# Optimization experiments

Hardware: AMD Instinct MI355X
Metric: run time of the kernel (lower is better)

## Reference

```python
import jax, jax.numpy as jnp
import numpy as np

F = 16      # frames
NV = 4096   # visual points per frame
NT = 512    # tactile points per frame
M = 4096    # model points
SCALE = 0.1


def setup_inputs() -> dict:
    key = jax.random.key(0)
    ks = jax.random.split(key, 6)
    return {
        "state": jax.random.normal(ks[0], (6,), dtype=jnp.float32) * 0.1,
        "model_points": jax.random.normal(ks[1], (M, 3), dtype=jnp.float32),
        "visual_points": jax.random.normal(ks[2], (F, NV, 3), dtype=jnp.float32),
        "tactile_points": jax.random.normal(ks[3], (F, NT, 3), dtype=jnp.float32),
        "physics_pred_states": jax.random.normal(ks[4], (F, 12), dtype=jnp.float32) * 0.1,
        "delta_time": jax.random.uniform(ks[5], (F,), dtype=jnp.float32, minval=0.01, maxval=0.05),
    }


def _skew(a):
    z = jnp.zeros((), a.dtype)
    return jnp.array([[z, -a[2], a[1]],
                      [a[2], z, -a[0]],
                      [-a[1], a[0], z]])


def _rot_from_omega(omega, dt):
    # Rodrigues: R = I + sin(theta*dt) S + (1 - cos(theta*dt)) S@S, S = skew(omega/|omega|)
    theta = jnp.linalg.norm(omega)
    ax = omega / jnp.clip(theta, 1e-8)
    S = _skew(ax)
    return jnp.eye(3, dtype=omega.dtype) + jnp.sin(theta * dt) * S + (1.0 - jnp.cos(theta * dt)) * (S @ S)


def _chamfer(pred, gt):
    # rows: pred [N,3], cols: gt [M,3]; row-min of squared distances, then mean
    d = (jnp.sum(pred * pred, axis=1)[:, None]
         + jnp.sum(gt * gt, axis=1)[None, :]
         - 2.0 * pred @ gt.T)
    return jnp.mean(jnp.min(d, axis=1))


def reference(state, model_points, visual_points, tactile_points, physics_pred_states, delta_time):
    t0 = state[:3]
    r0 = _rot_from_omega(state[3:], jnp.float32(1.0))  # Euler2Mat modeled as axis-angle

    def pose_step(carry, x):
        t, r = carry
        v, omega, dt = x
        t = t + v * dt
        r = _rot_from_omega(omega, dt) @ r
        return (t, r), (t, r)

    _, (ts, rs) = jax.lax.scan(
        pose_step, (t0, r0),
        (physics_pred_states[1:, 6:9], physics_pred_states[1:, 9:12], delta_time[1:]))
    ts = jnp.concatenate([t0[None], ts], axis=0)  # [F,3]
    rs = jnp.concatenate([r0[None], rs], axis=0)  # [F,3,3]

    def frame_loss(acc, x):
        t, r, vp, tp = x
        vc = ((vp - t) @ r) / SCALE
        tc = ((tp - t) @ r) / SCALE
        acc = acc + _chamfer(vc, model_points) + 0.1 * _chamfer(tc, model_points)
        return acc, None

    E_cd, _ = jax.lax.scan(frame_loss, jnp.zeros((), jnp.float32),
                           (ts, rs, visual_points, tactile_points))
    return E_cd
```

## Files before the change

kernel.cpp:

```cpp
#include <hip/hip_runtime.h>
#include <math.h>

#define F_    16
#define NV_   4096
#define NT_   512
#define M_    4096
#define PPF_  (NV_ + NT_)
#define NPTS_ (F_ * PPF_)
#define SCALE_INV 10.0f

#define TPB    256
#define NPB    36
#define NCHUNK 32
#define CPM    128
#define PPT    8

#define PART_OFF (72 * 1024)

typedef float v2f __attribute__((ext_vector_type(2)));

__device__ inline void rot_from_omega(float ox, float oy, float oz, float dt,
                                      float* R) {
    float theta = sqrtf(ox * ox + oy * oy + oz * oz);
    float inv = 1.0f / fmaxf(theta, 1e-8f);
    float ax = ox * inv, ay = oy * inv, az = oz * inv;
    float s = sinf(theta * dt);
    float c = 1.0f - cosf(theta * dt);
    R[0] = 1.0f - c * (ay * ay + az * az);
    R[1] = -s * az + c * ax * ay;
    R[2] =  s * ay + c * ax * az;
    R[3] =  s * az + c * ax * ay;
    R[4] = 1.0f - c * (ax * ax + az * az);
    R[5] = -s * ax + c * ay * az;
    R[6] = -s * ay + c * ax * az;
    R[7] =  s * ax + c * ay * az;
    R[8] = 1.0f - c * (ax * ax + ay * ay);
}

__device__ __forceinline__ void pkdist2(v2f qa01, v2f qa23, v2f qb01, v2f qb23,
                                        const v2f* c0, const v2f* c1,
                                        const v2f* c2, float* dm) {
    v2f A0, A1, A2, A3, B0, B1, B2, B3;
    asm(
        "v_pk_fma_f32 %0, %9, %20, %9  op_sel:[0,0,1] op_sel_hi:[0,1,1]\n\t"
        "v_pk_fma_f32 %1, %9, %21, %9  op_sel:[0,0,1] op_sel_hi:[0,1,1]\n\t"
        "v_pk_fma_f32 %2, %9, %22, %9  op_sel:[0,0,1] op_sel_hi:[0,1,1]\n\t"
        "v_pk_fma_f32 %3, %9, %23, %9  op_sel:[0,0,1] op_sel_hi:[0,1,1]\n\t"
        "v_pk_fma_f32 %4, %11, %20, %11 op_sel:[0,0,1] op_sel_hi:[0,1,1]\n\t"
        "v_pk_fma_f32 %5, %11, %21, %11 op_sel:[0,0,1] op_sel_hi:[0,1,1]\n\t"
        "v_pk_fma_f32 %6, %11, %22, %11 op_sel:[0,0,1] op_sel_hi:[0,1,1]\n\t"
        "v_pk_fma_f32 %7, %11, %23, %11 op_sel:[0,0,1] op_sel_hi:[0,1,1]\n\t"
        "v_pk_fma_f32 %0, %8, %16, %0  op_sel:[1,0,0] op_sel_hi:[1,1,1]\n\t"
        "v_pk_fma_f32 %1, %8, %17, %1  op_sel:[1,0,0] op_sel_hi:[1,1,1]\n\t"
        "v_pk_fma_f32 %2, %8, %18, %2  op_sel:[1,0,0] op_sel_hi:[1,1,1]\n\t"
        "v_pk_fma_f32 %3, %8, %19, %3  op_sel:[1,0,0] op_sel_hi:[1,1,1]\n\t"
        "v_pk_fma_f32 %4, %10, %16, %4 op_sel:[1,0,0] op_sel_hi:[1,1,1]\n\t"
        "v_pk_fma_f32 %5, %10, %17, %5 op_sel:[1,0,0] op_sel_hi:[1,1,1]\n\t"
        "v_pk_fma_f32 %6, %10, %18, %6 op_sel:[1,0,0] op_sel_hi:[1,1,1]\n\t"
        "v_pk_fma_f32 %7, %10, %19, %7 op_sel:[1,0,0] op_sel_hi:[1,1,1]\n\t"
        "v_pk_fma_f32 %0, %8, %12, %0  op_sel:[0,0,0] op_sel_hi:[0,1,1]\n\t"
        "v_pk_fma_f32 %1, %8, %13, %1  op_sel:[0,0,0] op_sel_hi:[0,1,1]\n\t"
        "v_pk_fma_f32 %2, %8, %14, %2  op_sel:[0,0,0] op_sel_hi:[0,1,1]\n\t"
        "v_pk_fma_f32 %3, %8, %15, %3  op_sel:[0,0,0] op_sel_hi:[0,1,1]\n\t"
        "v_pk_fma_f32 %4, %10, %12, %4 op_sel:[0,0,0] op_sel_hi:[0,1,1]\n\t"
        "v_pk_fma_f32 %5, %10, %13, %5 op_sel:[0,0,0] op_sel_hi:[0,1,1]\n\t"
        "v_pk_fma_f32 %6, %10, %14, %6 op_sel:[0,0,0] op_sel_hi:[0,1,1]\n\t"
        "v_pk_fma_f32 %7, %10, %15, %7 op_sel:[0,0,0] op_sel_hi:[0,1,1]"
        : "=&v"(A0), "=&v"(A1), "=&v"(A2), "=&v"(A3),
          "=&v"(B0), "=&v"(B1), "=&v"(B2), "=&v"(B3)
        : "s"(qa01), "s"(qa23), "s"(qb01), "s"(qb23),
          "v"(c0[0]), "v"(c0[1]), "v"(c0[2]), "v"(c0[3]),
          "v"(c1[0]), "v"(c1[1]), "v"(c1[2]), "v"(c1[3]),
          "v"(c2[0]), "v"(c2[1]), "v"(c2[2]), "v"(c2[3]));
    dm[0] = fminf(fminf(A0.x, B0.x), dm[0]);
    dm[1] = fminf(fminf(A0.y, B0.y), dm[1]);
    dm[2] = fminf(fminf(A1.x, B1.x), dm[2]);
    dm[3] = fminf(fminf(A1.y, B1.y), dm[3]);
    dm[4] = fminf(fminf(A2.x, B2.x), dm[4]);
    dm[5] = fminf(fminf(A2.y, B2.y), dm[5]);
    dm[6] = fminf(fminf(A3.x, B3.x), dm[6]);
    dm[7] = fminf(fminf(A3.y, B3.y), dm[7]);
}

__global__ void prep_kernel(const float* __restrict__ state,
                            const float* __restrict__ phys,
                            const float* __restrict__ dts,
                            const float* __restrict__ model,
                            float* __restrict__ ws_pose,
                            float4* __restrict__ ws_feat) {
    const int b = blockIdx.x, t = threadIdx.x;
    if (b == 0) {
        __shared__ float sRs[F_ * 9];
        __shared__ float sdt[F_ * 3];
        if (t < F_) {
            float ox, oy, oz, dt;
            if (t == 0) { ox = state[3]; oy = state[4]; oz = state[5]; dt = 1.0f; }
            else        { ox = phys[t * 12 + 9]; oy = phys[t * 12 + 10];
                          oz = phys[t * 12 + 11]; dt = dts[t]; }
            float Rs[9];
            rot_from_omega(ox, oy, oz, dt, Rs);
            for (int j = 0; j < 9; ++j) sRs[t * 9 + j] = Rs[j];
            if (t > 0) {
                sdt[t * 3 + 0] = phys[t * 12 + 6] * dt;
                sdt[t * 3 + 1] = phys[t * 12 + 7] * dt;
                sdt[t * 3 + 2] = phys[t * 12 + 8] * dt;
            }
        }
        if (t == 0) {
            float R[9];
            for (int j = 0; j < 9; ++j) R[j] = sRs[j];
            float tr[3] = {state[0], state[1], state[2]};
            for (int i = 0; i < F_; ++i) {
                if (i > 0) {
                    tr[0] += sdt[i * 3 + 0];
                    tr[1] += sdt[i * 3 + 1];
                    tr[2] += sdt[i * 3 + 2];
                    float Rn[9];
                    const float* Rsp = sRs + i * 9;
                    for (int r = 0; r < 3; ++r)
                        for (int c2 = 0; c2 < 3; ++c2)
                            Rn[r * 3 + c2] = Rsp[r * 3 + 0] * R[0 + c2] +
                                             Rsp[r * 3 + 1] * R[3 + c2] +
                                             Rsp[r * 3 + 2] * R[6 + c2];
                    for (int j = 0; j < 9; ++j) R[j] = Rn[j];
                }
                float* o = ws_pose + i * 12;
                o[0] = tr[0]; o[1] = tr[1]; o[2] = tr[2];
                for (int j = 0; j < 9; ++j) o[3 + j] = R[j] * SCALE_INV;
            }
        }
    } else {
        const int id = (b - 1) * 256 + t;
        float gx = model[id * 3 + 0], gy = model[id * 3 + 1], gz = model[id * 3 + 2];
        ws_feat[id] = make_float4(-2.0f * gx, -2.0f * gy, -2.0f * gz,
                                  gx * gx + gy * gy + gz * gz);
    }
}

__global__ __launch_bounds__(TPB, 4) void chamfer_main(
    const float* __restrict__ vis, const float* __restrict__ tac,
    const float* __restrict__ ws_pose, const float4* __restrict__ ws_feat,
    float* __restrict__ partials) {
    __shared__ float spose[F_ * 12];
    const int t  = threadIdx.x;
    const int pb = blockIdx.x;
    const int ch = blockIdx.y;

    if (t < F_ * 12) spose[t] = ws_pose[t];
    __syncthreads();

    v2f c0p[4], c1p[4], c2p[4];
    float cn[PPT], dm[PPT];
#pragma unroll
    for (int k = 0; k < PPT; ++k) {
        int pt  = pb * 2048 + k * 256 + t;
        int f   = pt / PPF_;
        int loc = pt - f * PPF_;
        const float* p = (loc < NV_) ? (vis + ((size_t)f * NV_ + loc) * 3)
                                     : (tac + ((size_t)f * NT_ + (loc - NV_)) * 3);
        const float* ps = spose + f * 12;
        float d0 = p[0] - ps[0], d1 = p[1] - ps[1], d2 = p[2] - ps[2];
        const float* R = ps + 3;
        float x = d0 * R[0] + d1 * R[3] + d2 * R[6];
        float y = d0 * R[1] + d1 * R[4] + d2 * R[7];
        float z = d0 * R[2] + d1 * R[5] + d2 * R[8];
        cn[k] = x * x + y * y + z * z;
        dm[k] = 3.4e38f;
        if (k & 1) { c0p[k >> 1].y = x; c1p[k >> 1].y = y; c2p[k >> 1].y = z; }
        else       { c0p[k >> 1].x = x; c1p[k >> 1].x = y; c2p[k >> 1].x = z; }
    }

    const v2f* fch = (const v2f*)(ws_feat + (size_t)ch * CPM);
#pragma unroll 4
    for (int m = 0; m < CPM; m += 2) {
        v2f qa01 = fch[2 * m + 0];
        v2f qa23 = fch[2 * m + 1];
        v2f qb01 = fch[2 * m + 2];
        v2f qb23 = fch[2 * m + 3];
        pkdist2(qa01, qa23, qb01, qb23, c0p, c1p, c2p, dm);
    }

#pragma unroll
    for (int k = 0; k < PPT; ++k)
        partials[(size_t)ch * NPTS_ + pb * 2048 + k * 256 + t] = dm[k] + cn[k];
}

__global__ __launch_bounds__(TPB) void chamfer_reduce(
    const float* __restrict__ partials, float* __restrict__ out) {
    __shared__ float sw[TPB / 64];
    const int pt = blockIdx.x * TPB + threadIdx.x;
    float m = partials[pt];
    for (int ch = 1; ch < NCHUNK; ++ch)
        m = fminf(m, partials[(size_t)ch * NPTS_ + pt]);
    const int loc = pt % PPF_;
    const float w = (loc < NV_) ? (1.0f / NV_) : (0.1f / NT_);
    float v = m * w;
#pragma unroll
    for (int off = 32; off > 0; off >>= 1) v += __shfl_down(v, off);
    if ((threadIdx.x & 63) == 0) sw[threadIdx.x >> 6] = v;
    __syncthreads();
    if (threadIdx.x == 0) {
        float s = 0.0f;
        for (int i = 0; i < TPB / 64; ++i) s += sw[i];
        atomicAdd(out, s);
    }
}

__global__ __launch_bounds__(TPB) void chamfer_fb(
    const float* __restrict__ state, const float* __restrict__ model,
    const float* __restrict__ vis, const float* __restrict__ tac,
    const float* __restrict__ phys, const float* __restrict__ dts,
    float* __restrict__ out) {
    __shared__ float sw[4];
    const int pt = blockIdx.x * TPB + threadIdx.x;
    const int f = pt / PPF_, loc = pt - f * PPF_;
    float R[9], tr[3] = {state[0], state[1], state[2]};
    rot_from_omega(state[3], state[4], state[5], 1.0f, R);
    for (int i = 1; i <= f; ++i) {
        float dt = dts[i];
        tr[0] += phys[i * 12 + 6] * dt;
        tr[1] += phys[i * 12 + 7] * dt;
        tr[2] += phys[i * 12 + 8] * dt;
        float Rs[9], Rn[9];
        rot_from_omega(phys[i * 12 + 9], phys[i * 12 + 10], phys[i * 12 + 11], dt, Rs);
        for (int r = 0; r < 3; ++r)
            for (int c2 = 0; c2 < 3; ++c2)
                Rn[r * 3 + c2] = Rs[r * 3 + 0] * R[0 + c2] +
                                 Rs[r * 3 + 1] * R[3 + c2] +
                                 Rs[r * 3 + 2] * R[6 + c2];
        for (int j = 0; j < 9; ++j) R[j] = Rn[j];
    }
    for (int j = 0; j < 9; ++j) R[j] *= SCALE_INV;
    const float* p = (loc < NV_) ? (vis + ((size_t)f * NV_ + loc) * 3)
                                 : (tac + ((size_t)f * NT_ + (loc - NV_)) * 3);
    float d0 = p[0] - tr[0], d1 = p[1] - tr[1], d2 = p[2] - tr[2];
    float x = d0 * R[0] + d1 * R[3] + d2 * R[6];
    float y = d0 * R[1] + d1 * R[4] + d2 * R[7];
    float z = d0 * R[2] + d1 * R[5] + d2 * R[8];
    float cn = x * x + y * y + z * z;
    float mn = 3.4e38f;
    for (int i = 0; i < M_; ++i) {
        float gx = model[i * 3], gy = model[i * 3 + 1], gz = model[i * 3 + 2];
        float gn = gx * gx + gy * gy + gz * gz;
        float dd = fmaf(-2.0f * gx, x, fmaf(-2.0f * gy, y, fmaf(-2.0f * gz, z, gn)));
        mn = fminf(mn, dd);
    }
    float w = (loc < NV_) ? (1.0f / NV_) : (0.1f / NT_);
    float v = (mn + cn) * w;
    for (int off = 32; off > 0; off >>= 1) v += __shfl_down(v, off);
    if ((threadIdx.x & 63) == 0) sw[threadIdx.x >> 6] = v;
    __syncthreads();
    if (threadIdx.x == 0) atomicAdd(out, sw[0] + sw[1] + sw[2] + sw[3]);
}

extern "C" void kernel_launch(void* const* d_in, const int* in_sizes, int n_in,
                              void* d_out, int out_size, void* d_ws, size_t ws_size,
                              hipStream_t stream) {
    const float* state = (const float*)d_in[0];
    const float* model = (const float*)d_in[1];
    const float* vis   = (const float*)d_in[2];
    const float* tac   = (const float*)d_in[3];
    const float* phys  = (const float*)d_in[4];
    const float* dts   = (const float*)d_in[5];
    float* out = (float*)d_out;

    const size_t NEED = PART_OFF + (size_t)NCHUNK * NPTS_ * sizeof(float);
    hipMemsetAsync(out, 0, sizeof(float), stream);
    if (ws_size >= NEED) {
        float*  ws_pose  = (float*)d_ws;
        float4* ws_feat  = (float4*)((char*)d_ws + 1024);
        float*  partials = (float*)((char*)d_ws + PART_OFF);
        prep_kernel<<<17, 256, 0, stream>>>(state, phys, dts, model, ws_pose, ws_feat);
        dim3 grid(NPB, NCHUNK);
        chamfer_main<<<grid, TPB, 0, stream>>>(vis, tac, ws_pose, ws_feat, partials);
        chamfer_reduce<<<NPTS_ / TPB, TPB, 0, stream>>>(partials, out);
    } else {
        chamfer_fb<<<NPTS_ / TPB, TPB, 0, stream>>>(state, model, vis, tac, phys,
                                                    dts, out);
    }
}
```

Baseline: 107.4 us.

## Fuse chamfer min reduction into main kernel via per-block shared-memory min

Reorganises the main kernel so each block handles 32 points of one frame, with 32 thread groups each scanning a 128-point slice of the model. Per-group minima are combined in shared memory and summed with an atomic, which removes the global partials buffer and the separate reduce kernel. Model features now live in VGPRs, not SGPRs, since each lane group reads a different slice, and each thread holds 4 points instead of 8, which cuts register reuse of each model load. Occupancy is raised to 8 blocks per CU and the grid grows to 2304 blocks, so there are more atomics on the output.

```diff
diff --git a/kernel.cpp b/kernel.cpp
--- a/kernel.cpp
+++ b/kernel.cpp
@@ -9,15 +9,15 @@
 #define NPTS_ (F_ * PPF_)
 #define SCALE_INV 10.0f
 
-#define TPB    256
-#define NPB    36
-#define NCHUNK 32
-#define CPM    128
-#define PPT    8
-
-#define PART_OFF (72 * 1024)
+#define TPB   256
+#define PTSB  32
+#define NBLK  (NPTS_ / PTSB)
+#define NGR   32
+#define MPG   (M_ / NGR)
+#define PPL   4
 
 typedef float v2f __attribute__((ext_vector_type(2)));
+typedef float v4f __attribute__((ext_vector_type(4)));
 
 __device__ inline void rot_from_omega(float ox, float oy, float oz, float dt,
                                       float* R) {
@@ -37,49 +37,29 @@
     R[8] = 1.0f - c * (ax * ax + ay * ay);
 }
 
-__device__ __forceinline__ void pkdist2(v2f qa01, v2f qa23, v2f qb01, v2f qb23,
-                                        const v2f* c0, const v2f* c1,
-                                        const v2f* c2, float* dm) {
-    v2f A0, A1, A2, A3, B0, B1, B2, B3;
-    asm(
-        "v_pk_fma_f32 %0, %9, %20, %9  op_sel:[0,0,1] op_sel_hi:[0,1,1]\n\t"
-        "v_pk_fma_f32 %1, %9, %21, %9  op_sel:[0,0,1] op_sel_hi:[0,1,1]\n\t"
-        "v_pk_fma_f32 %2, %9, %22, %9  op_sel:[0,0,1] op_sel_hi:[0,1,1]\n\t"
-        "v_pk_fma_f32 %3, %9, %23, %9  op_sel:[0,0,1] op_sel_hi:[0,1,1]\n\t"
-        "v_pk_fma_f32 %4, %11, %20, %11 op_sel:[0,0,1] op_sel_hi:[0,1,1]\n\t"
-        "v_pk_fma_f32 %5, %11, %21, %11 op_sel:[0,0,1] op_sel_hi:[0,1,1]\n\t"
-        "v_pk_fma_f32 %6, %11, %22, %11 op_sel:[0,0,1] op_sel_hi:[0,1,1]\n\t"
-        "v_pk_fma_f32 %7, %11, %23, %11 op_sel:[0,0,1] op_sel_hi:[0,1,1]\n\t"
-        "v_pk_fma_f32 %0, %8, %16, %0  op_sel:[1,0,0] op_sel_hi:[1,1,1]\n\t"
-        "v_pk_fma_f32 %1, %8, %17, %1  op_sel:[1,0,0] op_sel_hi:[1,1,1]\n\t"
-        "v_pk_fma_f32 %2, %8, %18, %2  op_sel:[1,0,0] op_sel_hi:[1,1,1]\n\t"
-        "v_pk_fma_f32 %3, %8, %19, %3  op_sel:[1,0,0] op_sel_hi:[1,1,1]\n\t"
-        "v_pk_fma_f32 %4, %10, %16, %4 op_sel:[1,0,0] op_sel_hi:[1,1,1]\n\t"
-        "v_pk_fma_f32 %5, %10, %17, %5 op_sel:[1,0,0] op_sel_hi:[1,1,1]\n\t"
-        "v_pk_fma_f32 %6, %10, %18, %6 op_sel:[1,0,0] op_sel_hi:[1,1,1]\n\t"
-        "v_pk_fma_f32 %7, %10, %19, %7 op_sel:[1,0,0] op_sel_hi:[1,1,1]\n\t"
-        "v_pk_fma_f32 %0, %8, %12, %0  op_sel:[0,0,0] op_sel_hi:[0,1,1]\n\t"
-        "v_pk_fma_f32 %1, %8, %13, %1  op_sel:[0,0,0] op_sel_hi:[0,1,1]\n\t"
-        "v_pk_fma_f32 %2, %8, %14, %2  op_sel:[0,0,0] op_sel_hi:[0,1,1]\n\t"
-        "v_pk_fma_f32 %3, %8, %15, %3  op_sel:[0,0,0] op_sel_hi:[0,1,1]\n\t"
-        "v_pk_fma_f32 %4, %10, %12, %4 op_sel:[0,0,0] op_sel_hi:[0,1,1]\n\t"
-        "v_pk_fma_f32 %5, %10, %13, %5 op_sel:[0,0,0] op_sel_hi:[0,1,1]\n\t"
-        "v_pk_fma_f32 %6, %10, %14, %6 op_sel:[0,0,0] op_sel_hi:[0,1,1]\n\t"
-        "v_pk_fma_f32 %7, %10, %15, %7 op_sel:[0,0,0] op_sel_hi:[0,1,1]"
-        : "=&v"(A0), "=&v"(A1), "=&v"(A2), "=&v"(A3),
-          "=&v"(B0), "=&v"(B1), "=&v"(B2), "=&v"(B3)
-        : "s"(qa01), "s"(qa23), "s"(qb01), "s"(qb23),
-          "v"(c0[0]), "v"(c0[1]), "v"(c0[2]), "v"(c0[3]),
-          "v"(c1[0]), "v"(c1[1]), "v"(c1[2]), "v"(c1[3]),
-          "v"(c2[0]), "v"(c2[1]), "v"(c2[2]), "v"(c2[3]));
+__device__ __forceinline__ void pkdist1(v2f qa01, v2f qa23, v2f qb01, v2f qb23,
+                                        v2f c0p0, v2f c0p1, v2f c1p0, v2f c1p1,
+                                        v2f c2p0, v2f c2p1, float* dm) {
+    v2f A0, A1, B0, B1;
+    asm("v_pk_fma_f32 %0, %5, %12, %5 op_sel:[0,0,1] op_sel_hi:[0,1,1]\n\t"
+        "v_pk_fma_f32 %1, %5, %13, %5 op_sel:[0,0,1] op_sel_hi:[0,1,1]\n\t"
+        "v_pk_fma_f32 %2, %7, %12, %7 op_sel:[0,0,1] op_sel_hi:[0,1,1]\n\t"
+        "v_pk_fma_f32 %3, %7, %13, %7 op_sel:[0,0,1] op_sel_hi:[0,1,1]\n\t"
+        "v_pk_fma_f32 %0, %4, %10, %0 op_sel:[1,0,0] op_sel_hi:[1,1,1]\n\t"
+        "v_pk_fma_f32 %1, %4, %11, %1 op_sel:[1,0,0] op_sel_hi:[1,1,1]\n\t"
+        "v_pk_fma_f32 %2, %6, %10, %2 op_sel:[1,0,0] op_sel_hi:[1,1,1]\n\t"
+        "v_pk_fma_f32 %3, %6, %11, %3 op_sel:[1,0,0] op_sel_hi:[1,1,1]\n\t"
+        "v_pk_fma_f32 %0, %4, %8, %0  op_sel:[0,0,0] op_sel_hi:[0,1,1]\n\t"
+        "v_pk_fma_f32 %1, %4, %9, %1  op_sel:[0,0,0] op_sel_hi:[0,1,1]\n\t"
+        "v_pk_fma_f32 %2, %6, %8, %2  op_sel:[0,0,0] op_sel_hi:[0,1,1]\n\t"
+        "v_pk_fma_f32 %3, %6, %9, %3  op_sel:[0,0,0] op_sel_hi:[0,1,1]"
+        : "=&v"(A0), "=&v"(A1), "=&v"(B0), "=&v"(B1)
+        : "v"(qa01), "v"(qa23), "v"(qb01), "v"(qb23),
+          "v"(c0p0), "v"(c0p1), "v"(c1p0), "v"(c1p1), "v"(c2p0), "v"(c2p1));
     dm[0] = fminf(fminf(A0.x, B0.x), dm[0]);
     dm[1] = fminf(fminf(A0.y, B0.y), dm[1]);
     dm[2] = fminf(fminf(A1.x, B1.x), dm[2]);
     dm[3] = fminf(fminf(A1.y, B1.y), dm[3]);
-    dm[4] = fminf(fminf(A2.x, B2.x), dm[4]);
-    dm[5] = fminf(fminf(A2.y, B2.y), dm[5]);
-    dm[6] = fminf(fminf(A3.x, B3.x), dm[6]);
-    dm[7] = fminf(fminf(A3.y, B3.y), dm[7]);
 }
 
 __global__ void prep_kernel(const float* __restrict__ state,
@@ -137,72 +117,79 @@
     }
 }
 
-__global__ __launch_bounds__(TPB, 4) void chamfer_main(
+__global__ __launch_bounds__(TPB, 8) void chamfer_main(
     const float* __restrict__ vis, const float* __restrict__ tac,
     const float* __restrict__ ws_pose, const float4* __restrict__ ws_feat,
-    float* __restrict__ partials) {
+    float* __restrict__ out) {
     __shared__ float spose[F_ * 12];
+    __shared__ float sdm[PTSB][NGR + 1];
+
     const int t  = threadIdx.x;
-    const int pb = blockIdx.x;
-    const int ch = blockIdx.y;
+    const int g  = t >> 3;
+    const int pl = t & 7;
+    const int f  = blockIdx.x / 144;
+    const int lbase = (blockIdx.x - f * 144) * PTSB;
 
     if (t < F_ * 12) spose[t] = ws_pose[t];
     __syncthreads();
 
-    v2f c0p[4], c1p[4], c2p[4];
-    float cn[PPT], dm[PPT];
-#pragma unroll
-    for (int k = 0; k < PPT; ++k) {
-        int pt  = pb * 2048 + k * 256 + t;
-        int f   = pt / PPF_;
-        int loc = pt - f * PPF_;
-        const float* p = (loc < NV_) ? (vis + ((size_t)f * NV_ + loc) * 3)
-                                     : (tac + ((size_t)f * NT_ + (loc - NV_)) * 3);
+    v2f c0p[2], c1p[2], c2p[2];
+    float cn[PPL], dm[PPL];
+    {
         const float* ps = spose + f * 12;
-        float d0 = p[0] - ps[0], d1 = p[1] - ps[1], d2 = p[2] - ps[2];
-        const float* R = ps + 3;
-        float x = d0 * R[0] + d1 * R[3] + d2 * R[6];
-        float y = d0 * R[1] + d1 * R[4] + d2 * R[7];
-        float z = d0 * R[2] + d1 * R[5] + d2 * R[8];
-        cn[k] = x * x + y * y + z * z;
-        dm[k] = 3.4e38f;
-        if (k & 1) { c0p[k >> 1].y = x; c1p[k >> 1].y = y; c2p[k >> 1].y = z; }
-        else       { c0p[k >> 1].x = x; c1p[k >> 1].x = y; c2p[k >> 1].x = z; }
-    }
-
-    const v2f* fch = (const v2f*)(ws_feat + (size_t)ch * CPM);
-#pragma unroll 4
-    for (int m = 0; m < CPM; m += 2) {
-        v2f qa01 = fch[2 * m + 0];
-        v2f qa23 = fch[2 * m + 1];
-        v2f qb01 = fch[2 * m + 2];
-        v2f qb23 = fch[2 * m + 3];
-        pkdist2(qa01, qa23, qb01, qb23, c0p, c1p, c2p, dm);
-    }
-
-#pragma unroll
-    for (int k = 0; k < PPT; ++k)
-        partials[(size_t)ch * NPTS_ + pb * 2048 + k * 256 + t] = dm[k] + cn[k];
-}
-
-__global__ __launch_bounds__(TPB) void chamfer_reduce(
-    const float* __restrict__ partials, float* __restrict__ out) {
-    __shared__ float sw[TPB / 64];
-    const int pt = blockIdx.x * TPB + threadIdx.x;
-    float m = partials[pt];
-    for (int ch = 1; ch < NCHUNK; ++ch)
-        m = fminf(m, partials[(size_t)ch * NPTS_ + pt]);
-    const int loc = pt % PPF_;
-    const float w = (loc < NV_) ? (1.0f / NV_) : (0.1f / NT_);
-    float v = m * w;
-#pragma unroll
-    for (int off = 32; off > 0; off >>= 1) v += __shfl_down(v, off);
-    if ((threadIdx.x & 63) == 0) sw[threadIdx.x >> 6] = v;
+        float xx[PPL], yy[PPL], zz[PPL];
+#pragma unroll
+        for (int k = 0; k < PPL; ++k) {
+            int loc = lbase + pl * PPL + k;
+            const float* p = (loc < NV_) ? (vis + ((size_t)f * NV_ + loc) * 3)
+                                         : (tac + ((size_t)f * NT_ + (loc - NV_)) * 3);
+            float d0 = p[0] - ps[0], d1 = p[1] - ps[1], d2 = p[2] - ps[2];
+            const float* R = ps + 3;
+            float x = d0 * R[0] + d1 * R[3] + d2 * R[6];
+            float y = d0 * R[1] + d1 * R[4] + d2 * R[7];
+            float z = d0 * R[2] + d1 * R[5] + d2 * R[8];
+            xx[k] = x; yy[k] = y; zz[k] = z;
+            cn[k] = x * x + y * y + z * z;
+            dm[k] = 3.4e38f;
+        }
+#pragma unroll
+        for (int j = 0; j < 2; ++j) {
+            c0p[j] = (v2f){xx[2 * j], xx[2 * j + 1]};
+            c1p[j] = (v2f){yy[2 * j], yy[2 * j + 1]};
+            c2p[j] = (v2f){zz[2 * j], zz[2 * j + 1]};
+        }
+    }
+
+    const v4f* fg = (const v4f*)(ws_feat + (size_t)g * MPG);
+#pragma unroll 2
+    for (int m = 0; m < MPG; m += 2) {
+        v4f ga = fg[m];
+        v4f gb = fg[m + 1];
+        pkdist1(__builtin_shufflevector(ga, ga, 0, 1),
+                __builtin_shufflevector(ga, ga, 2, 3),
+                __builtin_shufflevector(gb, gb, 0, 1),
+                __builtin_shufflevector(gb, gb, 2, 3),
+                c0p[0], c0p[1], c1p[0], c1p[1], c2p[0], c2p[1], dm);
+    }
+
+#pragma unroll
+    for (int k = 0; k < PPL; ++k) sdm[pl * PPL + k][g] = dm[k] + cn[k];
     __syncthreads();
-    if (threadIdx.x == 0) {
-        float s = 0.0f;
-        for (int i = 0; i < TPB / 64; ++i) s += sw[i];
-        atomicAdd(out, s);
+
+    if (t < 64) {
+        float v = 0.0f;
+        if (t < PTSB) {
+            const float* row = sdm[t];
+            float mn = row[0];
+#pragma unroll 8
+            for (int i = 1; i < NGR; ++i) mn = fminf(mn, row[i]);
+            const int loc = lbase + t;
+            const float w = (loc < NV_) ? (1.0f / NV_) : (0.1f / NT_);
+            v = mn * w;
+        }
+#pragma unroll
+        for (int off = 32; off > 0; off >>= 1) v += __shfl_down(v, off);
+        if (t == 0) atomicAdd(out, v);
     }
 }
 
@@ -237,7 +224,7 @@
     float x = d0 * R[0] + d1 * R[3] + d2 * R[6];
     float y = d0 * R[1] + d1 * R[4] + d2 * R[7];
     float z = d0 * R[2] + d1 * R[5] + d2 * R[8];
-    float cn = x * x + y * y + z * z;
+    float cnv = x * x + y * y + z * z;
     float mn = 3.4e38f;
     for (int i = 0; i < M_; ++i) {
         float gx = model[i * 3], gy = model[i * 3 + 1], gz = model[i * 3 + 2];
@@ -246,7 +233,7 @@
         mn = fminf(mn, dd);
     }
     float w = (loc < NV_) ? (1.0f / NV_) : (0.1f / NT_);
-    float v = (mn + cn) * w;
+    float v = (mn + cnv) * w;
     for (int off = 32; off > 0; off >>= 1) v += __shfl_down(v, off);
     if ((threadIdx.x & 63) == 0) sw[threadIdx.x >> 6] = v;
     __syncthreads();
@@ -264,16 +251,13 @@
     const float* dts   = (const float*)d_in[5];
     float* out = (float*)d_out;
 
-    const size_t NEED = PART_OFF + (size_t)NCHUNK * NPTS_ * sizeof(float);
+    const size_t NEED = 1024 + (size_t)M_ * sizeof(float4);
     hipMemsetAsync(out, 0, sizeof(float), stream);
     if (ws_size >= NEED) {
-        float*  ws_pose  = (float*)d_ws;
-        float4* ws_feat  = (float4*)((char*)d_ws + 1024);
-        float*  partials = (float*)((char*)d_ws + PART_OFF);
+        float*  ws_pose = (float*)d_ws;
+        float4* ws_feat = (float4*)((char*)d_ws + 1024);
         prep_kernel<<<17, 256, 0, stream>>>(state, phys, dts, model, ws_pose, ws_feat);
-        dim3 grid(NPB, NCHUNK);
-        chamfer_main<<<grid, TPB, 0, stream>>>(vis, tac, ws_pose, ws_feat, partials);
-        chamfer_reduce<<<NPTS_ / TPB, TPB, 0, stream>>>(partials, out);
+        chamfer_main<<<NBLK, TPB, 0, stream>>>(vis, tac, ws_pose, ws_feat, out);
     } else {
         chamfer_fb<<<NPTS_ / TPB, TPB, 0, stream>>>(state, model, vis, tac, phys,
                                                     dts, out);
```

After: 126.1 us. +17.4%, slower.
